# Optimization experiments

Measured on AMD Instinct MI355X. Metric: run time of the kernel, lower is better.

The kernel has to match this reference:

```python
import jax, jax.numpy as jnp
import numpy as np

N_NODES = 50000
N_EDGES = 800000
IN_F, HID, HEADS, OUT_F = 64, 64, 4, 64
NEG_SLOPE = 0.2


def _gat_conv(x, ei, W, a_src, a_dst, b, H, C):
    """PyG-style GATConv (eval mode, add_self_loops=True, concat=True).
    x: [N, F_in], ei: [2, E], W: [F_in, H*C], a_src/a_dst: [H, C], b: [H*C].
    """
    N = x.shape[0]
    h = (x @ W).reshape(N, H, C)                      # [N,H,C]
    asrc = jnp.einsum('nhc,hc->nh', h, a_src)         # [N,H]
    adst = jnp.einsum('nhc,hc->nh', h, a_dst)         # [N,H]
    src, dst = ei[0], ei[1]
    logits = jax.nn.leaky_relu(asrc[src] + adst[dst], NEG_SLOPE)  # [E,H]
    m = jax.ops.segment_max(logits, dst, num_segments=N)
    m = jnp.where(jnp.isfinite(m), m, 0.0)
    ex = jnp.exp(logits - m[dst])
    denom = jax.ops.segment_sum(ex, dst, num_segments=N)
    alpha = ex / (denom[dst] + 1e-16)                 # [E,H]
    msg = h[src] * alpha[:, :, None]                  # [E,H,C]
    out = jax.ops.segment_sum(msg, dst, num_segments=N)  # [N,H,C]
    return out.reshape(N, H * C) + b


def _add_self_loops(ei, n):
    loops = jnp.arange(n, dtype=ei.dtype)
    return jnp.concatenate([ei, jnp.stack([loops, loops])], axis=1)


def setup_inputs() -> dict:
    key = jax.random.key(0)
    ks = jax.random.split(key, 16)
    x = jax.random.normal(ks[0], (N_NODES, IN_F), dtype=jnp.float32)
    edge_index = jax.random.randint(ks[1], (2, N_EDGES), 0, N_NODES, dtype=jnp.int32)
    s = 0.1
    d = {'x': x, 'edge_index': edge_index}
    # layer 0: IN_F -> HID, HEADS heads
    d['W0'] = jax.random.normal(ks[2], (IN_F, HEADS * HID), jnp.float32) * s
    d['a_src0'] = jax.random.normal(ks[3], (HEADS, HID), jnp.float32) * s
    d['a_dst0'] = jax.random.normal(ks[4], (HEADS, HID), jnp.float32) * s
    d['b0'] = jnp.zeros((HEADS * HID,), jnp.float32)
    # layer 1: HEADS*HID -> HID, HEADS heads
    d['W1'] = jax.random.normal(ks[5], (HEADS * HID, HEADS * HID), jnp.float32) * s
    d['a_src1'] = jax.random.normal(ks[6], (HEADS, HID), jnp.float32) * s
    d['a_dst1'] = jax.random.normal(ks[7], (HEADS, HID), jnp.float32) * s
    d['b1'] = jnp.zeros((HEADS * HID,), jnp.float32)
    # layer 2: HEADS*HID -> OUT_F, 1 head
    d['W2'] = jax.random.normal(ks[8], (HEADS * HID, OUT_F), jnp.float32) * s
    d['a_src2'] = jax.random.normal(ks[9], (1, OUT_F), jnp.float32) * s
    d['a_dst2'] = jax.random.normal(ks[10], (1, OUT_F), jnp.float32) * s
    d['b2'] = jnp.zeros((OUT_F,), jnp.float32)
    return d


def reference(x, edge_index, W0, a_src0, a_dst0, b0, W1, a_src1, a_dst1, b1, W2, a_src2, a_dst2, b2):
    ei = _add_self_loops(edge_index, x.shape[0])
    h = _gat_conv(x, ei, W0, a_src0, a_dst0, b0, HEADS, HID)
    h = jax.nn.elu(h)  # dropout identity in eval
    h = _gat_conv(h, ei, W1, a_src1, a_dst1, b1, HEADS, HID)
    h = jax.nn.elu(h)
    out = _gat_conv(h, ei, W2, a_src2, a_dst2, b2, 1, OUT_F)
    return out
```

## Files before the change

kernel.cpp:

```cpp
#include <hip/hip_runtime.h>
#include <hip/hip_fp16.h>
#include <math.h>

#define NODES 50000
#define EDGES 800000
#define NB_SCAN ((NODES + 1023) / 1024)

typedef __attribute__((ext_vector_type(8))) _Float16 f16x8;
typedef __attribute__((ext_vector_type(4))) _Float16 f16x4;
typedef __attribute__((ext_vector_type(4))) float f32x4;

__device__ __forceinline__ float lrelu02(float x){ return x > 0.f ? x : 0.2f * x; }

__device__ __forceinline__ f32x4 shflx4(f32x4 v, int m){
  f32x4 r;
  r[0] = __shfl_xor(v[0], m); r[1] = __shfl_xor(v[1], m);
  r[2] = __shfl_xor(v[2], m); r[3] = __shfl_xor(v[3], m);
  return r;
}


__global__ __launch_bounds__(256) void gat_zero(int* __restrict__ p, int n){
  int i = blockIdx.x * 256 + threadIdx.x;
  if (i < n) p[i] = 0;
}

__global__ __launch_bounds__(256) void gat_hist(const int* __restrict__ ei, int* __restrict__ cnt){
  int e = blockIdx.x * 256 + threadIdx.x;
  if (e < EDGES) atomicAdd(&cnt[ei[EDGES + e]], 1);
}

__global__ __launch_bounds__(256) void gat_blocksum(const int* __restrict__ cnt, int* __restrict__ bsums){
  __shared__ int sd[256];
  int t = threadIdx.x, b = blockIdx.x;
  int base = b * 1024 + t * 4, s = 0;
  #pragma unroll
  for (int j = 0; j < 4; j++){ int i = base + j; if (i < NODES) s += cnt[i]; }
  sd[t] = s; __syncthreads();
  for (int o = 128; o > 0; o >>= 1){ if (t < o) sd[t] += sd[t + o]; __syncthreads(); }
  if (t == 0) bsums[b] = sd[0];
}

__global__ void gat_scan_bsums(int* bsums, int nb){
  if (threadIdx.x == 0 && blockIdx.x == 0){
    int run = 0;
    for (int i = 0; i < nb; i++){ int v = bsums[i]; bsums[i] = run; run += v; }
  }
}

__global__ __launch_bounds__(256) void gat_rowptr(int* __restrict__ cnt, const int* __restrict__ bsums,
                                                  int* __restrict__ row_ptr){
  __shared__ int sd[256];
  int t = threadIdx.x, b = blockIdx.x;
  int base = b * 1024 + t * 4;
  int c[4]; int s = 0;
  #pragma unroll
  for (int j = 0; j < 4; j++){
    int i = base + j;
    c[j] = (i < NODES) ? cnt[i] : 0;
    s += c[j];
    if (i < NODES) cnt[i] = 0;
  }
  sd[t] = s; __syncthreads();
  for (int o = 1; o < 256; o <<= 1){
    int v = (t >= o) ? sd[t - o] : 0;
    __syncthreads();
    if (t >= o) sd[t] += v;
    __syncthreads();
  }
  int off = bsums[b] + sd[t] - s;
  #pragma unroll
  for (int j = 0; j < 4; j++){
    int i = base + j;
    if (i < NODES){ row_ptr[i] = off; off += c[j]; }
  }
  if (b == 0 && t == 0) row_ptr[NODES] = EDGES;
}

__global__ __launch_bounds__(256) void gat_scatter(const int* __restrict__ ei, const int* __restrict__ row_ptr,
                                                    int* __restrict__ fill, int* __restrict__ col,
                                                    int* __restrict__ dstarr){
  int e = blockIdx.x * 256 + threadIdx.x;
  if (e < EDGES){
    int s = ei[e], d = ei[EDGES + e];
    int pos = row_ptr[d] + atomicAdd(&fill[d], 1);
    col[pos] = s;
    dstarr[pos] = d;
  }
}


__global__ __launch_bounds__(256) void gat_cvt_h(const float* __restrict__ src, _Float16* __restrict__ dst, int n4){
  int i = blockIdx.x * 256 + threadIdx.x;
  if (i < n4){
    float4 v = *(const float4*)(src + (size_t)i * 4);
    f16x4 h = { (_Float16)v.x, (_Float16)v.y, (_Float16)v.z, (_Float16)v.w };
    *(f16x4*)(dst + (size_t)i * 4) = h;
  }
}

__global__ __launch_bounds__(256) void gat_wt_all(const float* __restrict__ W0, const float* __restrict__ W1,
                                                  const float* __restrict__ W2,
                                                  _Float16* __restrict__ Wt0, _Float16* __restrict__ Wt1,
                                                  _Float16* __restrict__ Wt2){
  int n = threadIdx.x;
  int k = blockIdx.x;
  if (k < 64){
    Wt0[(size_t)n * 64 + k] = (_Float16)W0[(size_t)k * 256 + n];
  } else if (k < 320){
    int kk = k - 64;
    Wt1[(size_t)n * 256 + kk] = (_Float16)W1[(size_t)kk * 256 + n];
  } else {
    int kk = k - 320;
    if (n < 64) Wt2[(size_t)n * 256 + kk] = (_Float16)W2[(size_t)kk * 64 + n];
  }
}

__global__ __launch_bounds__(256) void gat_ws0(const float* __restrict__ W0, const float* __restrict__ a_src0,
                                               const float* __restrict__ a_dst0,
                                               float* __restrict__ ws, float* __restrict__ wd){
  int t = threadIdx.x;
  int h = t >> 6, c = t & 63;
  float s = 0.f, d = 0.f;
  for (int cc = 0; cc < 64; cc++){
    float w = W0[(size_t)c * 256 + h * 64 + cc];
    s += w * a_src0[h * 64 + cc];
    d += w * a_dst0[h * 64 + cc];
  }
  ws[h * 64 + c] = s;
  wd[h * 64 + c] = d;
}


template<int K, int N>
__global__ __launch_bounds__(256) void gat_gemm_mfma(const _Float16* __restrict__ A, const _Float16* __restrict__ Wt,
                                                      _Float16* __restrict__ C, int M){
  constexpr int NT = N / 64;
  constexpr int LDT = 40;
  __shared__ _Float16 As[64][LDT];
  __shared__ _Float16 Bs[N][LDT];

  int tid = threadIdx.x;
  int w = tid >> 6, l = tid & 63;
  int lg = l >> 4, lr = l & 15;
  int bm = blockIdx.x * 64;

  f32x4 acc[4][NT];
  #pragma unroll
  for (int m = 0; m < 4; m++)
    #pragma unroll
    for (int n = 0; n < NT; n++)
      acc[m][n] = (f32x4){0.f, 0.f, 0.f, 0.f};

  int ar = tid >> 2;
  int akc = (tid & 3) * 8;
  bool avalid = (bm + ar) < M;
  const _Float16* aptr = A + (size_t)(bm + ar) * K + akc;

  for (int k0 = 0; k0 < K; k0 += 32){
    float4 av = avalid ? *(const float4*)(aptr + k0) : make_float4(0.f, 0.f, 0.f, 0.f);
    __syncthreads();
    *(float4*)&As[ar][akc] = av;
    #pragma unroll
    for (int c = 0; c < N / 64; c++){
      int idx = c * 256 + tid;
      int n = idx >> 2, kc = (idx & 3) * 8;
      *(float4*)&Bs[n][kc] = *(const float4*)(Wt + (size_t)n * K + k0 + kc);
    }
    __syncthreads();

    f16x8 af[4], bf[NT];
    #pragma unroll
    for (int m = 0; m < 4; m++) af[m] = *(const f16x8*)&As[16 * m + lr][8 * lg];
    #pragma unroll
    for (int n = 0; n < NT; n++) bf[n] = *(const f16x8*)&Bs[w * (N / 4) + 16 * n + lr][8 * lg];
    #pragma unroll
    for (int m = 0; m < 4; m++)
      #pragma unroll
      for (int n = 0; n < NT; n++)
        acc[m][n] = __builtin_amdgcn_mfma_f32_16x16x32_f16(af[m], bf[n], acc[m][n], 0, 0, 0);
  }

  #pragma unroll
  for (int m = 0; m < 4; m++){
    #pragma unroll
    for (int j = 0; j < 4; j++){
      int row = bm + 16 * m + 4 * lg + j;
      if (row < M){
        #pragma unroll
        for (int n = 0; n < NT; n++)
          C[(size_t)row * N + w * (N / 4) + 16 * n + lr] = (_Float16)acc[m][n][j];
      }
    }
  }
}


__global__ __launch_bounds__(256) void gat_gemm_bd(const _Float16* __restrict__ A, const _Float16* __restrict__ Bt,
                                                    const float* __restrict__ bias, _Float16* __restrict__ C, int M){
  int tid = threadIdx.x;
  int w = tid >> 6, l = tid & 63;
  int lg = l >> 4, lr = l & 15;
  int bm = blockIdx.x * 64;

  f32x4 acc[4][4];
  #pragma unroll
  for (int m = 0; m < 4; m++)
    #pragma unroll
    for (int n = 0; n < 4; n++)
      acc[m][n] = (f32x4){0.f, 0.f, 0.f, 0.f};

  f16x8 zf = {};
  #pragma unroll
  for (int ks = 0; ks < 2; ks++){
    int koff = ks * 32;
    f16x8 af[4], bf[4];
    #pragma unroll
    for (int m = 0; m < 4; m++){
      int row = bm + 16 * m + lr;
      af[m] = (row < M) ? *(const f16x8*)(A + (size_t)row * 256 + w * 64 + koff + 8 * lg) : zf;
    }
    #pragma unroll
    for (int n = 0; n < 4; n++)
      bf[n] = *(const f16x8*)(Bt + (size_t)(w * 64 + 16 * n + lr) * 64 + koff + 8 * lg);
    #pragma unroll
    for (int m = 0; m < 4; m++)
      #pragma unroll
      for (int n = 0; n < 4; n++)
        acc[m][n] = __builtin_amdgcn_mfma_f32_16x16x32_f16(af[m], bf[n], acc[m][n], 0, 0, 0);
  }

  #pragma unroll
  for (int m = 0; m < 4; m++){
    #pragma unroll
    for (int j = 0; j < 4; j++){
      int row = bm + 16 * m + 4 * lg + j;
      if (row < M){
        #pragma unroll
        for (int n = 0; n < 4; n++){
          int cc = w * 64 + 16 * n + lr;
          float o = acc[m][n][j] + bias[cc];
          o = o > 0.f ? o : expm1f(o);
          C[(size_t)row * 256 + cc] = (_Float16)o;
        }
      }
    }
  }
}


__global__ __launch_bounds__(256) void gat_attn0(const _Float16* __restrict__ xh, const float* __restrict__ ws,
                                                  const float* __restrict__ wd,
                                                  float* __restrict__ asrc, float* __restrict__ adst, int N){
  int lane = threadIdx.x & 63;
  int wid = threadIdx.x >> 6;
  int n = blockIdx.x * 4 + wid;
  if (n >= N) return;
  float v = (float)xh[(size_t)n * 64 + lane];
  #pragma unroll
  for (int h = 0; h < 4; h++){
    float s1 = v * ws[h * 64 + lane];
    float s2 = v * wd[h * 64 + lane];
    #pragma unroll
    for (int o = 32; o > 0; o >>= 1){ s1 += __shfl_xor(s1, o); s2 += __shfl_xor(s2, o); }
    if (lane == 0){ asrc[n * 4 + h] = s1; adst[n * 4 + h] = s2; }
  }
}

__global__ __launch_bounds__(256) void gat_attn4(const _Float16* __restrict__ h, const float* __restrict__ a_src,
                                                  const float* __restrict__ a_dst,
                                                  float* __restrict__ asrc, float* __restrict__ adst, int N){
  int lane = threadIdx.x & 63;
  int wid = threadIdx.x >> 6;
  int n = blockIdx.x * 4 + wid;
  if (n >= N) return;
  int co = lane * 4;
  f16x4 hv = *(const f16x4*)(h + (size_t)n * 256 + co);
  float4 av = *(const float4*)&a_src[co];
  float4 dv = *(const float4*)&a_dst[co];
  float f0 = (float)hv[0], f1 = (float)hv[1], f2 = (float)hv[2], f3 = (float)hv[3];
  float s1 = f0 * av.x + f1 * av.y + f2 * av.z + f3 * av.w;
  float s2 = f0 * dv.x + f1 * dv.y + f2 * dv.z + f3 * dv.w;
  #pragma unroll
  for (int o = 8; o > 0; o >>= 1){ s1 += __shfl_xor(s1, o); s2 += __shfl_xor(s2, o); }
  if ((lane & 15) == 0){
    int q = lane >> 4;
    asrc[n * 4 + q] = s1;
    adst[n * 4 + q] = s2;
  }
}

__global__ __launch_bounds__(256) void gat_attn1(const _Float16* __restrict__ h, const float* __restrict__ a_src,
                                                  const float* __restrict__ a_dst,
                                                  float* __restrict__ asrc, float* __restrict__ adst, int N){
  int lane = threadIdx.x & 63;
  int wid = threadIdx.x >> 6;
  int n = blockIdx.x * 4 + wid;
  if (n >= N) return;
  float v = (float)h[(size_t)n * 64 + lane];
  float s1 = v * a_src[lane];
  float s2 = v * a_dst[lane];
  #pragma unroll
  for (int o = 32; o > 0; o >>= 1){ s1 += __shfl_xor(s1, o); s2 += __shfl_xor(s2, o); }
  if (lane == 0){ asrc[n] = s1; adst[n] = s2; }
}


__global__ __launch_bounds__(256) void gat_edge_exp0(const int* __restrict__ col, const int* __restrict__ dstarr,
                                                      const float* __restrict__ asrc, const float* __restrict__ adst,
                                                      float* __restrict__ exf){
  int i = blockIdx.x * 256 + threadIdx.x;
  if (i >= EDGES) return;
  int s = col[i], d = dstarr[i];
  float4 a = *(const float4*)&asrc[s * 4];
  float4 b = *(const float4*)&adst[d * 4];
  float4 r;
  r.x = __expf(lrelu02(a.x + b.x));
  r.y = __expf(lrelu02(a.y + b.y));
  r.z = __expf(lrelu02(a.z + b.z));
  r.w = __expf(lrelu02(a.w + b.w));
  *(float4*)&exf[(size_t)i * 4] = r;
}

__global__ __launch_bounds__(256) void gat_edge_exp1h(const int* __restrict__ col, const int* __restrict__ dstarr,
                                                       const float* __restrict__ asrc, const float* __restrict__ adst,
                                                       float* __restrict__ exf1){
  int i = blockIdx.x * 256 + threadIdx.x;
  if (i >= EDGES) return;
  exf1[i] = __expf(lrelu02(asrc[col[i]] + adst[dstarr[i]]));
}


__global__ __launch_bounds__(256) void gat_aggregate_in64(const _Float16* __restrict__ xh, const float* __restrict__ exf,
                                                           const float* __restrict__ asrc, const float* __restrict__ adst,
                                                           const int* __restrict__ row_ptr, const int* __restrict__ col,
                                                           _Float16* __restrict__ agg){
  int lane = threadIdx.x & 63;
  int wid = threadIdx.x >> 6;
  int d = blockIdx.x * 4 + wid;
  if (d >= NODES) return;
  int slot = lane >> 4;
  int cpos = (lane & 15) * 4;

  f32x4 acc0 = {0,0,0,0}, acc1 = {0,0,0,0}, acc2 = {0,0,0,0}, acc3 = {0,0,0,0};
  f32x4 den = {0,0,0,0};

  int e0 = row_ptr[d], e1 = row_ptr[d + 1];
  const _Float16* xb = xh + cpos;
  int e = e0;
  for (; e + 8 <= e1; e += 8){
    int eA = e + slot, eB = e + 4 + slot;
    int sA = col[eA], sB = col[eB];
    float4 fA = *(const float4*)(exf + (size_t)eA * 4);
    float4 fB = *(const float4*)(exf + (size_t)eB * 4);
    f16x4 hA = *(const f16x4*)(xb + (size_t)sA * 64);
    f16x4 hB = *(const f16x4*)(xb + (size_t)sB * 64);
    f32x4 vA = { (float)hA[0], (float)hA[1], (float)hA[2], (float)hA[3] };
    f32x4 vB = { (float)hB[0], (float)hB[1], (float)hB[2], (float)hB[3] };
    den += (f32x4){ fA.x + fB.x, fA.y + fB.y, fA.z + fB.z, fA.w + fB.w };
    acc0 += fA.x * vA + fB.x * vB;
    acc1 += fA.y * vA + fB.y * vB;
    acc2 += fA.z * vA + fB.z * vB;
    acc3 += fA.w * vA + fB.w * vB;
  }
  if (e + 4 <= e1){
    int eA = e + slot;
    int sA = col[eA];
    float4 fA = *(const float4*)(exf + (size_t)eA * 4);
    f16x4 hA = *(const f16x4*)(xb + (size_t)sA * 64);
    f32x4 vA = { (float)hA[0], (float)hA[1], (float)hA[2], (float)hA[3] };
    den += (f32x4){ fA.x, fA.y, fA.z, fA.w };
    acc0 += fA.x * vA; acc1 += fA.y * vA; acc2 += fA.z * vA; acc3 += fA.w * vA;
    e += 4;
  }
  {
    int eA = e + slot;
    if (eA < e1){
      int sA = col[eA];
      float4 fA = *(const float4*)(exf + (size_t)eA * 4);
      f16x4 hA = *(const f16x4*)(xb + (size_t)sA * 64);
      f32x4 vA = { (float)hA[0], (float)hA[1], (float)hA[2], (float)hA[3] };
      den += (f32x4){ fA.x, fA.y, fA.z, fA.w };
      acc0 += fA.x * vA; acc1 += fA.y * vA; acc2 += fA.z * vA; acc3 += fA.w * vA;
    }
  }

  #pragma unroll
  for (int off = 16; off <= 32; off <<= 1){
    acc0 += shflx4(acc0, off);
    acc1 += shflx4(acc1, off);
    acc2 += shflx4(acc2, off);
    acc3 += shflx4(acc3, off);
    den  += shflx4(den,  off);
  }

  float4 a4 = *(const float4*)&asrc[d * 4];
  float4 b4 = *(const float4*)&adst[d * 4];
  float es0 = __expf(lrelu02(a4.x + b4.x));
  float es1 = __expf(lrelu02(a4.y + b4.y));
  float es2 = __expf(lrelu02(a4.z + b4.z));
  float es3 = __expf(lrelu02(a4.w + b4.w));
  f16x4 hs = *(const f16x4*)(xh + (size_t)d * 64 + cpos);
  f32x4 vs = { (float)hs[0], (float)hs[1], (float)hs[2], (float)hs[3] };
  acc0 += es0 * vs; acc1 += es1 * vs; acc2 += es2 * vs; acc3 += es3 * vs;
  den += (f32x4){ es0, es1, es2, es3 };

  if (slot == 0){
    float i0 = 1.f / (den[0] + 1e-16f), i1 = 1.f / (den[1] + 1e-16f);
    float i2 = 1.f / (den[2] + 1e-16f), i3 = 1.f / (den[3] + 1e-16f);
    _Float16* ob = agg + (size_t)d * 256 + cpos;
    f16x4 o0 = { (_Float16)(acc0[0]*i0), (_Float16)(acc0[1]*i0), (_Float16)(acc0[2]*i0), (_Float16)(acc0[3]*i0) };
    f16x4 o1 = { (_Float16)(acc1[0]*i1), (_Float16)(acc1[1]*i1), (_Float16)(acc1[2]*i1), (_Float16)(acc1[3]*i1) };
    f16x4 o2 = { (_Float16)(acc2[0]*i2), (_Float16)(acc2[1]*i2), (_Float16)(acc2[2]*i2), (_Float16)(acc2[3]*i2) };
    f16x4 o3 = { (_Float16)(acc3[0]*i3), (_Float16)(acc3[1]*i3), (_Float16)(acc3[2]*i3), (_Float16)(acc3[3]*i3) };
    *(f16x4*)(ob)       = o0;
    *(f16x4*)(ob + 64)  = o1;
    *(f16x4*)(ob + 128) = o2;
    *(f16x4*)(ob + 192) = o3;
  }
}


__global__ __launch_bounds__(256) void gat_aggregate4(const _Float16* __restrict__ hH, const float* __restrict__ asrc,
                                                       const float* __restrict__ adst,
                                                       const int* __restrict__ row_ptr, const int* __restrict__ col,
                                                       const float* __restrict__ bias, _Float16* __restrict__ out){
  int lane = threadIdx.x & 63;
  int wid = threadIdx.x >> 6;
  int d = blockIdx.x * 4 + wid;
  if (d >= NODES) return;
  int q = lane >> 4;
  int co = lane * 4;

  float adq = adst[d * 4 + q];

  float ex = __expf(lrelu02(asrc[d * 4 + q] + adq));
  f16x4 hv = *(const f16x4*)(hH + (size_t)d * 256 + co);
  float4 acc = make_float4(ex * (float)hv[0], ex * (float)hv[1], ex * (float)hv[2], ex * (float)hv[3]);
  float den = ex;

  int e0 = row_ptr[d], e1 = row_ptr[d + 1];
  const _Float16* hbase = hH + co;
  int e = e0;
  for (; e < e1 && (e & 3); e++){
    int s0 = col[e];
    float a0 = asrc[s0 * 4 + q];
    f16x4 h0 = *(const f16x4*)(hbase + (size_t)s0 * 256);
    float x0 = __expf(lrelu02(a0 + adq));
    den += x0;
    acc.x += x0 * (float)h0[0]; acc.y += x0 * (float)h0[1];
    acc.z += x0 * (float)h0[2]; acc.w += x0 * (float)h0[3];
  }
  for (; e + 8 <= e1; e += 8){
    int4 cA = *(const int4*)&col[e];
    int4 cB = *(const int4*)&col[e + 4];
    float a0 = asrc[cA.x * 4 + q], a1 = asrc[cA.y * 4 + q], a2 = asrc[cA.z * 4 + q], a3 = asrc[cA.w * 4 + q];
    float a4 = asrc[cB.x * 4 + q], a5 = asrc[cB.y * 4 + q], a6 = asrc[cB.z * 4 + q], a7 = asrc[cB.w * 4 + q];
    f16x4 h0 = *(const f16x4*)(hbase + (size_t)cA.x * 256);
    f16x4 h1 = *(const f16x4*)(hbase + (size_t)cA.y * 256);
    f16x4 h2 = *(const f16x4*)(hbase + (size_t)cA.z * 256);
    f16x4 h3 = *(const f16x4*)(hbase + (size_t)cA.w * 256);
    f16x4 h4 = *(const f16x4*)(hbase + (size_t)cB.x * 256);
    f16x4 h5 = *(const f16x4*)(hbase + (size_t)cB.y * 256);
    f16x4 h6 = *(const f16x4*)(hbase + (size_t)cB.z * 256);
    f16x4 h7 = *(const f16x4*)(hbase + (size_t)cB.w * 256);
    float x0 = __expf(lrelu02(a0 + adq)), x1 = __expf(lrelu02(a1 + adq));
    float x2 = __expf(lrelu02(a2 + adq)), x3 = __expf(lrelu02(a3 + adq));
    float x4 = __expf(lrelu02(a4 + adq)), x5 = __expf(lrelu02(a5 + adq));
    float x6 = __expf(lrelu02(a6 + adq)), x7 = __expf(lrelu02(a7 + adq));
    den += x0 + x1 + x2 + x3 + x4 + x5 + x6 + x7;
    acc.x += x0 * (float)h0[0] + x1 * (float)h1[0] + x2 * (float)h2[0] + x3 * (float)h3[0]
           + x4 * (float)h4[0] + x5 * (float)h5[0] + x6 * (float)h6[0] + x7 * (float)h7[0];
    acc.y += x0 * (float)h0[1] + x1 * (float)h1[1] + x2 * (float)h2[1] + x3 * (float)h3[1]
           + x4 * (float)h4[1] + x5 * (float)h5[1] + x6 * (float)h6[1] + x7 * (float)h7[1];
    acc.z += x0 * (float)h0[2] + x1 * (float)h1[2] + x2 * (float)h2[2] + x3 * (float)h3[2]
           + x4 * (float)h4[2] + x5 * (float)h5[2] + x6 * (float)h6[2] + x7 * (float)h7[2];
    acc.w += x0 * (float)h0[3] + x1 * (float)h1[3] + x2 * (float)h2[3] + x3 * (float)h3[3]
           + x4 * (float)h4[3] + x5 * (float)h5[3] + x6 * (float)h6[3] + x7 * (float)h7[3];
  }
  for (; e < e1; e++){
    int s0 = col[e];
    float a0 = asrc[s0 * 4 + q];
    f16x4 h0 = *(const f16x4*)(hbase + (size_t)s0 * 256);
    float x0 = __expf(lrelu02(a0 + adq));
    den += x0;
    acc.x += x0 * (float)h0[0]; acc.y += x0 * (float)h0[1];
    acc.z += x0 * (float)h0[2]; acc.w += x0 * (float)h0[3];
  }

  float inv = 1.f / (den + 1e-16f);
  float4 b4 = *(const float4*)&bias[co];
  float4 o = make_float4(acc.x * inv + b4.x, acc.y * inv + b4.y, acc.z * inv + b4.z, acc.w * inv + b4.w);
  o.x = o.x > 0.f ? o.x : expm1f(o.x);
  o.y = o.y > 0.f ? o.y : expm1f(o.y);
  o.z = o.z > 0.f ? o.z : expm1f(o.z);
  o.w = o.w > 0.f ? o.w : expm1f(o.w);
  f16x4 oh = { (_Float16)o.x, (_Float16)o.y, (_Float16)o.z, (_Float16)o.w };
  *(f16x4*)(out + (size_t)d * 256 + co) = oh;
}


__global__ __launch_bounds__(256) void gat_aggregate1n(const _Float16* __restrict__ hH, const float* __restrict__ exf1,
                                                        const float* __restrict__ asrc, const float* __restrict__ adst,
                                                        const int* __restrict__ row_ptr, const int* __restrict__ col,
                                                        const float* __restrict__ bias, float* __restrict__ out){
  int lane = threadIdx.x & 63;
  int wid = threadIdx.x >> 6;
  int d = blockIdx.x * 4 + wid;
  if (d >= NODES) return;
  int slot = lane >> 4;
  int cpos = (lane & 15) * 4;

  f32x4 acc = {0,0,0,0};
  float den = 0.f;

  int e0 = row_ptr[d], e1 = row_ptr[d + 1];
  const _Float16* hb = hH + cpos;
  int e = e0;
  for (; e + 8 <= e1; e += 8){
    int eA = e + slot, eB = e + 4 + slot;
    int sA = col[eA], sB = col[eB];
    float fA = exf1[eA], fB = exf1[eB];
    f16x4 hA = *(const f16x4*)(hb + (size_t)sA * 64);
    f16x4 hB = *(const f16x4*)(hb + (size_t)sB * 64);
    f32x4 vA = { (float)hA[0], (float)hA[1], (float)hA[2], (float)hA[3] };
    f32x4 vB = { (float)hB[0], (float)hB[1], (float)hB[2], (float)hB[3] };
    den += fA + fB;
    acc += fA * vA + fB * vB;
  }
  if (e + 4 <= e1){
    int eA = e + slot;
    int sA = col[eA];
    float fA = exf1[eA];
    f16x4 hA = *(const f16x4*)(hb + (size_t)sA * 64);
    f32x4 vA = { (float)hA[0], (float)hA[1], (float)hA[2], (float)hA[3] };
    den += fA; acc += fA * vA;
    e += 4;
  }
  {
    int eA = e + slot;
    if (eA < e1){
      int sA = col[eA];
      float fA = exf1[eA];
      f16x4 hA = *(const f16x4*)(hb + (size_t)sA * 64);
      f32x4 vA = { (float)hA[0], (float)hA[1], (float)hA[2], (float)hA[3] };
      den += fA; acc += fA * vA;
    }
  }

  #pragma unroll
  for (int off = 16; off <= 32; off <<= 1){
    acc += shflx4(acc, off);
    den += __shfl_xor(den, off);
  }

  float es = __expf(lrelu02(asrc[d] + adst[d]));
  f16x4 hs = *(const f16x4*)(hH + (size_t)d * 64 + cpos);
  f32x4 vs = { (float)hs[0], (float)hs[1], (float)hs[2], (float)hs[3] };
  acc += es * vs;
  den += es;

  if (slot == 0){
    float inv = 1.f / (den + 1e-16f);
    float4 b4 = *(const float4*)&bias[cpos];
    float4 o = make_float4(acc[0] * inv + b4.x, acc[1] * inv + b4.y, acc[2] * inv + b4.z, acc[3] * inv + b4.w);
    *(float4*)(out + (size_t)d * 64 + cpos) = o;
  }
}


extern "C" void kernel_launch(void* const* d_in, const int* in_sizes, int n_in,
                              void* d_out, int out_size, void* d_ws, size_t ws_size,
                              hipStream_t stream) {
  const float* x   = (const float*)d_in[0];
  const int*   ei  = (const int*)  d_in[1];
  const float* W0  = (const float*)d_in[2];
  const float* as0 = (const float*)d_in[3];
  const float* ad0 = (const float*)d_in[4];
  const float* b0  = (const float*)d_in[5];
  const float* W1  = (const float*)d_in[6];
  const float* as1 = (const float*)d_in[7];
  const float* ad1 = (const float*)d_in[8];
  const float* b1  = (const float*)d_in[9];
  const float* W2  = (const float*)d_in[10];
  const float* as2 = (const float*)d_in[11];
  const float* ad2 = (const float*)d_in[12];
  const float* b2  = (const float*)d_in[13];
  float* out = (float*)d_out;

  auto al = [](size_t v){ return (v + 255) & ~(size_t)255; };
  char* p = (char*)d_ws;
  int*      row_ptr = (int*)p;      p += al((NODES + 1) * sizeof(int));
  int*      cnt     = (int*)p;      p += al(NODES * sizeof(int));
  int*      bsums   = (int*)p;      p += al(64 * sizeof(int));
  int*      col     = (int*)p;      p += al(EDGES * sizeof(int));
  int*      dstarr  = (int*)p;      p += al(EDGES * sizeof(int));
  float*    exf     = (float*)p;    p += al((size_t)EDGES * 4 * sizeof(float));
  float*    asrc    = (float*)p;    p += al(NODES * 4 * sizeof(float));
  float*    adst    = (float*)p;    p += al(NODES * 4 * sizeof(float));
  _Float16* xh      = (_Float16*)p; p += al((size_t)NODES * 64 * sizeof(_Float16));
  _Float16* hH      = (_Float16*)p; p += al((size_t)NODES * 256 * sizeof(_Float16));
  _Float16* actb    = (_Float16*)p; p += al((size_t)NODES * 256 * sizeof(_Float16));
  _Float16* Wt0     = (_Float16*)p; p += al(256 * 64 * sizeof(_Float16));
  _Float16* Wt1     = (_Float16*)p; p += al(256 * 256 * sizeof(_Float16));
  _Float16* Wt2     = (_Float16*)p; p += al(64 * 256 * sizeof(_Float16));
  float*    ws0     = (float*)p;    p += al(256 * sizeof(float));
  float*    wd0     = (float*)p;    p += al(256 * sizeof(float));

  gat_cvt_h<<<(NODES * 64 / 4 + 255) / 256, 256, 0, stream>>>(x, xh, NODES * 64 / 4);
  gat_wt_all<<<576, 256, 0, stream>>>(W0, W1, W2, Wt0, Wt1, Wt2);
  gat_ws0<<<1, 256, 0, stream>>>(W0, as0, ad0, ws0, wd0);

  gat_zero<<<(NODES + 255) / 256, 256, 0, stream>>>(cnt, NODES);
  gat_hist<<<(EDGES + 255) / 256, 256, 0, stream>>>(ei, cnt);
  gat_blocksum<<<NB_SCAN, 256, 0, stream>>>(cnt, bsums);
  gat_scan_bsums<<<1, 64, 0, stream>>>(bsums, NB_SCAN);
  gat_rowptr<<<NB_SCAN, 256, 0, stream>>>(cnt, bsums, row_ptr);
  gat_scatter<<<(EDGES + 255) / 256, 256, 0, stream>>>(ei, row_ptr, cnt, col, dstarr);

  const int nodeBlocks = (NODES + 3) / 4;
  const int gemmBlocks = (NODES + 63) / 64;
  const int edgeBlocks = (EDGES + 255) / 256;

  gat_attn0<<<nodeBlocks, 256, 0, stream>>>(xh, ws0, wd0, asrc, adst, NODES);
  gat_edge_exp0<<<edgeBlocks, 256, 0, stream>>>(col, dstarr, asrc, adst, exf);
  gat_aggregate_in64<<<nodeBlocks, 256, 0, stream>>>(xh, exf, asrc, adst, row_ptr, col, hH);
  gat_gemm_bd<<<gemmBlocks, 256, 0, stream>>>(hH, Wt0, b0, actb, NODES);

  gat_gemm_mfma<256, 256><<<gemmBlocks, 256, 0, stream>>>(actb, Wt1, hH, NODES);
  gat_attn4<<<nodeBlocks, 256, 0, stream>>>(hH, as1, ad1, asrc, adst, NODES);
  gat_aggregate4<<<nodeBlocks, 256, 0, stream>>>(hH, asrc, adst, row_ptr, col, b1, actb);

  gat_gemm_mfma<256, 64><<<gemmBlocks, 256, 0, stream>>>(actb, Wt2, hH, NODES);
  gat_attn1<<<nodeBlocks, 256, 0, stream>>>(hH, as2, ad2, asrc, adst, NODES);
  gat_edge_exp1h<<<edgeBlocks, 256, 0, stream>>>(col, dstarr, asrc, adst, exf);
  gat_aggregate1n<<<nodeBlocks, 256, 0, stream>>>(hH, exf, asrc, adst, row_ptr, col, b2, out);
}
```

Before: 373.4 us.

## Fuse attention-score projections into GEMM epilogues and merge prep kernels

Computes the per-node source/destination attention scores for layers 1 and 2 inside the MFMA GEMM epilogue from the fp32 accumulators. This removes the separate attn4/attn1 kernels that re-read the GEMM output. The layer-2 edge-exp kernel is dropped and the exponentials are computed inline in the final aggregation. The three prep kernels are merged into one launch, and the layer-1 aggregation loop is simplified to a 4-wide unroll without alignment handling, which reduces memory-level parallelism per iteration.

```diff
diff --git a/kernel.cpp b/kernel.cpp
--- a/kernel.cpp
+++ b/kernel.cpp
@@ -90,51 +90,50 @@
 }
 
 
-__global__ __launch_bounds__(256) void gat_cvt_h(const float* __restrict__ src, _Float16* __restrict__ dst, int n4){
-  int i = blockIdx.x * 256 + threadIdx.x;
-  if (i < n4){
-    float4 v = *(const float4*)(src + (size_t)i * 4);
+__global__ __launch_bounds__(256) void gat_prep(const float* __restrict__ x, _Float16* __restrict__ xh,
+                                                const float* __restrict__ W0, const float* __restrict__ W1,
+                                                const float* __restrict__ W2,
+                                                _Float16* __restrict__ Wt0, _Float16* __restrict__ Wt1,
+                                                _Float16* __restrict__ Wt2,
+                                                const float* __restrict__ as0, const float* __restrict__ ad0,
+                                                float* __restrict__ ws, float* __restrict__ wd){
+  int b = blockIdx.x;
+  int t = threadIdx.x;
+  if (b < 3125){
+    int i = b * 256 + t;
+    float4 v = *(const float4*)(x + (size_t)i * 4);
     f16x4 h = { (_Float16)v.x, (_Float16)v.y, (_Float16)v.z, (_Float16)v.w };
-    *(f16x4*)(dst + (size_t)i * 4) = h;
-  }
-}
-
-__global__ __launch_bounds__(256) void gat_wt_all(const float* __restrict__ W0, const float* __restrict__ W1,
-                                                  const float* __restrict__ W2,
-                                                  _Float16* __restrict__ Wt0, _Float16* __restrict__ Wt1,
-                                                  _Float16* __restrict__ Wt2){
-  int n = threadIdx.x;
-  int k = blockIdx.x;
-  if (k < 64){
-    Wt0[(size_t)n * 64 + k] = (_Float16)W0[(size_t)k * 256 + n];
-  } else if (k < 320){
-    int kk = k - 64;
-    Wt1[(size_t)n * 256 + kk] = (_Float16)W1[(size_t)kk * 256 + n];
+    *(f16x4*)(xh + (size_t)i * 4) = h;
+  } else if (b < 3701){
+    int k = b - 3125;
+    if (k < 64){
+      Wt0[(size_t)t * 64 + k] = (_Float16)W0[(size_t)k * 256 + t];
+    } else if (k < 320){
+      int kk = k - 64;
+      Wt1[(size_t)t * 256 + kk] = (_Float16)W1[(size_t)kk * 256 + t];
+    } else {
+      int kk = k - 320;
+      if (t < 64) Wt2[(size_t)t * 256 + kk] = (_Float16)W2[(size_t)kk * 64 + t];
+    }
   } else {
-    int kk = k - 320;
-    if (n < 64) Wt2[(size_t)n * 256 + kk] = (_Float16)W2[(size_t)kk * 64 + n];
-  }
-}
-
-__global__ __launch_bounds__(256) void gat_ws0(const float* __restrict__ W0, const float* __restrict__ a_src0,
-                                               const float* __restrict__ a_dst0,
-                                               float* __restrict__ ws, float* __restrict__ wd){
-  int t = threadIdx.x;
-  int h = t >> 6, c = t & 63;
-  float s = 0.f, d = 0.f;
-  for (int cc = 0; cc < 64; cc++){
-    float w = W0[(size_t)c * 256 + h * 64 + cc];
-    s += w * a_src0[h * 64 + cc];
-    d += w * a_dst0[h * 64 + cc];
-  }
-  ws[h * 64 + c] = s;
-  wd[h * 64 + c] = d;
-}
-
-
-template<int K, int N>
+    int h = t >> 6, c = t & 63;
+    float s = 0.f, d = 0.f;
+    for (int cc = 0; cc < 64; cc++){
+      float w = W0[(size_t)c * 256 + h * 64 + cc];
+      s += w * as0[h * 64 + cc];
+      d += w * ad0[h * 64 + cc];
+    }
+    ws[h * 64 + c] = s;
+    wd[h * 64 + c] = d;
+  }
+}
+
+
+template<int K, int N, int ATTN>
 __global__ __launch_bounds__(256) void gat_gemm_mfma(const _Float16* __restrict__ A, const _Float16* __restrict__ Wt,
-                                                      _Float16* __restrict__ C, int M){
+                                                      _Float16* __restrict__ C,
+                                                      const float* __restrict__ a_srcv, const float* __restrict__ a_dstv,
+                                                      float* __restrict__ asrc, float* __restrict__ adst, int M){
   constexpr int NT = N / 64;
   constexpr int LDT = 40;
   __shared__ _Float16 As[64][LDT];
@@ -190,6 +189,56 @@
         #pragma unroll
         for (int n = 0; n < NT; n++)
           C[(size_t)row * N + w * (N / 4) + 16 * n + lr] = (_Float16)acc[m][n][j];
+      }
+    }
+  }
+
+  if constexpr (ATTN == 4){
+    float avs[4], avd[4];
+    #pragma unroll
+    for (int n = 0; n < 4; n++){
+      avs[n] = a_srcv[w * 64 + 16 * n + lr];
+      avd[n] = a_dstv[w * 64 + 16 * n + lr];
+    }
+    #pragma unroll
+    for (int m = 0; m < 4; m++){
+      #pragma unroll
+      for (int j = 0; j < 4; j++){
+        float s1 = acc[m][0][j] * avs[0] + acc[m][1][j] * avs[1] + acc[m][2][j] * avs[2] + acc[m][3][j] * avs[3];
+        float s2 = acc[m][0][j] * avd[0] + acc[m][1][j] * avd[1] + acc[m][2][j] * avd[2] + acc[m][3][j] * avd[3];
+        #pragma unroll
+        for (int o = 8; o > 0; o >>= 1){ s1 += __shfl_xor(s1, o); s2 += __shfl_xor(s2, o); }
+        int row = bm + 16 * m + 4 * lg + j;
+        if (lr == 0 && row < M){
+          asrc[row * 4 + w] = s1;
+          adst[row * 4 + w] = s2;
+        }
+      }
+    }
+  }
+  if constexpr (ATTN == 1){
+    __shared__ float sred[2][4][64];
+    float av = a_srcv[w * 16 + lr], dv = a_dstv[w * 16 + lr];
+    #pragma unroll
+    for (int m = 0; m < 4; m++){
+      #pragma unroll
+      for (int j = 0; j < 4; j++){
+        float s1 = acc[m][0][j] * av;
+        float s2 = acc[m][0][j] * dv;
+        #pragma unroll
+        for (int o = 8; o > 0; o >>= 1){ s1 += __shfl_xor(s1, o); s2 += __shfl_xor(s2, o); }
+        if (lr == 0){
+          sred[0][w][16 * m + 4 * lg + j] = s1;
+          sred[1][w][16 * m + 4 * lg + j] = s2;
+        }
+      }
+    }
+    __syncthreads();
+    if (tid < 64){
+      int row = bm + tid;
+      if (row < M){
+        asrc[row] = sred[0][0][tid] + sred[0][1][tid] + sred[0][2][tid] + sred[0][3][tid];
+        adst[row] = sred[1][0][tid] + sred[1][1][tid] + sred[1][2][tid] + sred[1][3][tid];
       }
     }
   }
@@ -265,44 +314,6 @@
     for (int o = 32; o > 0; o >>= 1){ s1 += __shfl_xor(s1, o); s2 += __shfl_xor(s2, o); }
     if (lane == 0){ asrc[n * 4 + h] = s1; adst[n * 4 + h] = s2; }
   }
-}
-
-__global__ __launch_bounds__(256) void gat_attn4(const _Float16* __restrict__ h, const float* __restrict__ a_src,
-                                                  const float* __restrict__ a_dst,
-                                                  float* __restrict__ asrc, float* __restrict__ adst, int N){
-  int lane = threadIdx.x & 63;
-  int wid = threadIdx.x >> 6;
-  int n = blockIdx.x * 4 + wid;
-  if (n >= N) return;
-  int co = lane * 4;
-  f16x4 hv = *(const f16x4*)(h + (size_t)n * 256 + co);
-  float4 av = *(const float4*)&a_src[co];
-  float4 dv = *(const float4*)&a_dst[co];
-  float f0 = (float)hv[0], f1 = (float)hv[1], f2 = (float)hv[2], f3 = (float)hv[3];
-  float s1 = f0 * av.x + f1 * av.y + f2 * av.z + f3 * av.w;
-  float s2 = f0 * dv.x + f1 * dv.y + f2 * dv.z + f3 * dv.w;
-  #pragma unroll
-  for (int o = 8; o > 0; o >>= 1){ s1 += __shfl_xor(s1, o); s2 += __shfl_xor(s2, o); }
-  if ((lane & 15) == 0){
-    int q = lane >> 4;
-    asrc[n * 4 + q] = s1;
-    adst[n * 4 + q] = s2;
-  }
-}
-
-__global__ __launch_bounds__(256) void gat_attn1(const _Float16* __restrict__ h, const float* __restrict__ a_src,
-                                                  const float* __restrict__ a_dst,
-                                                  float* __restrict__ asrc, float* __restrict__ adst, int N){
-  int lane = threadIdx.x & 63;
-  int wid = threadIdx.x >> 6;
-  int n = blockIdx.x * 4 + wid;
-  if (n >= N) return;
-  float v = (float)h[(size_t)n * 64 + lane];
-  float s1 = v * a_src[lane];
-  float s2 = v * a_dst[lane];
-  #pragma unroll
-  for (int o = 32; o > 0; o >>= 1){ s1 += __shfl_xor(s1, o); s2 += __shfl_xor(s2, o); }
-  if (lane == 0){ asrc[n] = s1; adst[n] = s2; }
 }
 
 
@@ -320,14 +331,6 @@
   r.z = __expf(lrelu02(a.z + b.z));
   r.w = __expf(lrelu02(a.w + b.w));
   *(float4*)&exf[(size_t)i * 4] = r;
-}
-
-__global__ __launch_bounds__(256) void gat_edge_exp1h(const int* __restrict__ col, const int* __restrict__ dstarr,
-                                                       const float* __restrict__ asrc, const float* __restrict__ adst,
-                                                       float* __restrict__ exf1){
-  int i = blockIdx.x * 256 + threadIdx.x;
-  if (i >= EDGES) return;
-  exf1[i] = __expf(lrelu02(asrc[col[i]] + adst[dstarr[i]]));
 }
 
 
@@ -442,41 +445,22 @@
   int e0 = row_ptr[d], e1 = row_ptr[d + 1];
   const _Float16* hbase = hH + co;
   int e = e0;
-  for (; e < e1 && (e & 3); e++){
-    int s0 = col[e];
-    float a0 = asrc[s0 * 4 + q];
+  for (; e + 4 <= e1; e += 4){
+    int s0 = col[e], s1 = col[e + 1], s2 = col[e + 2], s3 = col[e + 3];
+    float a0 = asrc[s0 * 4 + q], a1 = asrc[s1 * 4 + q], a2 = asrc[s2 * 4 + q], a3 = asrc[s3 * 4 + q];
     f16x4 h0 = *(const f16x4*)(hbase + (size_t)s0 * 256);
+    f16x4 h1 = *(const f16x4*)(hbase + (size_t)s1 * 256);
+    f16x4 h2 = *(const f16x4*)(hbase + (size_t)s2 * 256);
+    f16x4 h3 = *(const f16x4*)(hbase + (size_t)s3 * 256);
     float x0 = __expf(lrelu02(a0 + adq));
-    den += x0;
-    acc.x += x0 * (float)h0[0]; acc.y += x0 * (float)h0[1];
-    acc.z += x0 * (float)h0[2]; acc.w += x0 * (float)h0[3];
-  }
-  for (; e + 8 <= e1; e += 8){
-    int4 cA = *(const int4*)&col[e];
-    int4 cB = *(const int4*)&col[e + 4];
-    float a0 = asrc[cA.x * 4 + q], a1 = asrc[cA.y * 4 + q], a2 = asrc[cA.z * 4 + q], a3 = asrc[cA.w * 4 + q];
-    float a4 = asrc[cB.x * 4 + q], a5 = asrc[cB.y * 4 + q], a6 = asrc[cB.z * 4 + q], a7 = asrc[cB.w * 4 + q];
-    f16x4 h0 = *(const f16x4*)(hbase + (size_t)cA.x * 256);
-    f16x4 h1 = *(const f16x4*)(hbase + (size_t)cA.y * 256);
-    f16x4 h2 = *(const f16x4*)(hbase + (size_t)cA.z * 256);
-    f16x4 h3 = *(const f16x4*)(hbase + (size_t)cA.w * 256);
-    f16x4 h4 = *(const f16x4*)(hbase + (size_t)cB.x * 256);
-    f16x4 h5 = *(const f16x4*)(hbase + (size_t)cB.y * 256);
-    f16x4 h6 = *(const f16x4*)(hbase + (size_t)cB.z * 256);
-    f16x4 h7 = *(const f16x4*)(hbase + (size_t)cB.w * 256);
-    float x0 = __expf(lrelu02(a0 + adq)), x1 = __expf(lrelu02(a1 + adq));
-    float x2 = __expf(lrelu02(a2 + adq)), x3 = __expf(lrelu02(a3 + adq));
-    float x4 = __expf(lrelu02(a4 + adq)), x5 = __expf(lrelu02(a5 + adq));
-    float x6 = __expf(lrelu02(a6 + adq)), x7 = __expf(lrelu02(a7 + adq));
-    den += x0 + x1 + x2 + x3 + x4 + x5 + x6 + x7;
-    acc.x += x0 * (float)h0[0] + x1 * (float)h1[0] + x2 * (float)h2[0] + x3 * (float)h3[0]
-           + x4 * (float)h4[0] + x5 * (float)h5[0] + x6 * (float)h6[0] + x7 * (float)h7[0];
-    acc.y += x0 * (float)h0[1] + x1 * (float)h1[1] + x2 * (float)h2[1] + x3 * (float)h3[1]
-           + x4 * (float)h4[1] + x5 * (float)h5[1] + x6 * (float)h6[1] + x7 * (float)h7[1];
-    acc.z += x0 * (float)h0[2] + x1 * (float)h1[2] + x2 * (float)h2[2] + x3 * (float)h3[2]
-           + x4 * (float)h4[2] + x5 * (float)h5[2] + x6 * (float)h6[2] + x7 * (float)h7[2];
-    acc.w += x0 * (float)h0[3] + x1 * (float)h1[3] + x2 * (float)h2[3] + x3 * (float)h3[3]
-           + x4 * (float)h4[3] + x5 * (float)h5[3] + x6 * (float)h6[3] + x7 * (float)h7[3];
+    float x1 = __expf(lrelu02(a1 + adq));
+    float x2 = __expf(lrelu02(a2 + adq));
+    float x3 = __expf(lrelu02(a3 + adq));
+    den += x0 + x1 + x2 + x3;
+    acc.x += x0 * (float)h0[0] + x1 * (float)h1[0] + x2 * (float)h2[0] + x3 * (float)h3[0];
+    acc.y += x0 * (float)h0[1] + x1 * (float)h1[1] + x2 * (float)h2[1] + x3 * (float)h3[1];
+    acc.z += x0 * (float)h0[2] + x1 * (float)h1[2] + x2 * (float)h2[2] + x3 * (float)h3[2];
+    acc.w += x0 * (float)h0[3] + x1 * (float)h1[3] + x2 * (float)h2[3] + x3 * (float)h3[3];
   }
   for (; e < e1; e++){
     int s0 = col[e];
@@ -500,7 +484,7 @@
 }
 
 
-__global__ __launch_bounds__(256) void gat_aggregate1n(const _Float16* __restrict__ hH, const float* __restrict__ exf1,
+__global__ __launch_bounds__(256) void gat_aggregate1n(const _Float16* __restrict__ hH,
                                                         const float* __restrict__ asrc, const float* __restrict__ adst,
                                                         const int* __restrict__ row_ptr, const int* __restrict__ col,
                                                         const float* __restrict__ bias, float* __restrict__ out){
@@ -511,6 +495,7 @@
   int slot = lane >> 4;
   int cpos = (lane & 15) * 4;
 
+  float adq = adst[d];
   f32x4 acc = {0,0,0,0};
   float den = 0.f;
 
@@ -520,7 +505,8 @@
   for (; e + 8 <= e1; e += 8){
     int eA = e + slot, eB = e + 4 + slot;
     int sA = col[eA], sB = col[eB];
-    float fA = exf1[eA], fB = exf1[eB];
+    float fA = __expf(lrelu02(asrc[sA] + adq));
+    float fB = __expf(lrelu02(asrc[sB] + adq));
     f16x4 hA = *(const f16x4*)(hb + (size_t)sA * 64);
     f16x4 hB = *(const f16x4*)(hb + (size_t)sB * 64);
     f32x4 vA = { (float)hA[0], (float)hA[1], (float)hA[2], (float)hA[3] };
@@ -531,7 +517,7 @@
   if (e + 4 <= e1){
     int eA = e + slot;
     int sA = col[eA];
-    float fA = exf1[eA];
+    float fA = __expf(lrelu02(asrc[sA] + adq));
     f16x4 hA = *(const f16x4*)(hb + (size_t)sA * 64);
     f32x4 vA = { (float)hA[0], (float)hA[1], (float)hA[2], (float)hA[3] };
     den += fA; acc += fA * vA;
@@ -541,7 +527,7 @@
     int eA = e + slot;
     if (eA < e1){
       int sA = col[eA];
-      float fA = exf1[eA];
+      float fA = __expf(lrelu02(asrc[sA] + adq));
       f16x4 hA = *(const f16x4*)(hb + (size_t)sA * 64);
       f32x4 vA = { (float)hA[0], (float)hA[1], (float)hA[2], (float)hA[3] };
       den += fA; acc += fA * vA;
@@ -554,7 +540,7 @@
     den += __shfl_xor(den, off);
   }
 
-  float es = __expf(lrelu02(asrc[d] + adst[d]));
+  float es = __expf(lrelu02(asrc[d] + adq));
   f16x4 hs = *(const f16x4*)(hH + (size_t)d * 64 + cpos);
   f32x4 vs = { (float)hs[0], (float)hs[1], (float)hs[2], (float)hs[3] };
   acc += es * vs;
@@ -607,9 +593,7 @@
   float*    ws0     = (float*)p;    p += al(256 * sizeof(float));
   float*    wd0     = (float*)p;    p += al(256 * sizeof(float));
 
-  gat_cvt_h<<<(NODES * 64 / 4 + 255) / 256, 256, 0, stream>>>(x, xh, NODES * 64 / 4);
-  gat_wt_all<<<576, 256, 0, stream>>>(W0, W1, W2, Wt0, Wt1, Wt2);
-  gat_ws0<<<1, 256, 0, stream>>>(W0, as0, ad0, ws0, wd0);
+  gat_prep<<<3702, 256, 0, stream>>>(x, xh, W0, W1, W2, Wt0, Wt1, Wt2, as0, ad0, ws0, wd0);
 
   gat_zero<<<(NODES + 255) / 256, 256, 0, stream>>>(cnt, NODES);
   gat_hist<<<(EDGES + 255) / 256, 256, 0, stream>>>(ei, cnt);
@@ -627,12 +611,9 @@
   gat_aggregate_in64<<<nodeBlocks, 256, 0, stream>>>(xh, exf, asrc, adst, row_ptr, col, hH);
   gat_gemm_bd<<<gemmBlocks, 256, 0, stream>>>(hH, Wt0, b0, actb, NODES);
 
-  gat_gemm_mfma<256, 256><<<gemmBlocks, 256, 0, stream>>>(actb, Wt1, hH, NODES);
-  gat_attn4<<<nodeBlocks, 256, 0, stream>>>(hH, as1, ad1, asrc, adst, NODES);
+  gat_gemm_mfma<256, 256, 4><<<gemmBlocks, 256, 0, stream>>>(actb, Wt1, hH, as1, ad1, asrc, adst, NODES);
   gat_aggregate4<<<nodeBlocks, 256, 0, stream>>>(hH, asrc, adst, row_ptr, col, b1, actb);
 
-  gat_gemm_mfma<256, 64><<<gemmBlocks, 256, 0, stream>>>(actb, Wt2, hH, NODES);
-  gat_attn1<<<nodeBlocks, 256, 0, stream>>>(hH, as2, ad2, asrc, adst, NODES);
-  gat_edge_exp1h<<<edgeBlocks, 256, 0, stream>>>(col, dstarr, asrc, adst, exf);
-  gat_aggregate1n<<<nodeBlocks, 256, 0, stream>>>(hH, exf, asrc, adst, row_ptr, col, b2, out);
-}
+  gat_gemm_mfma<256, 64, 1><<<gemmBlocks, 256, 0, stream>>>(actb, Wt2, hH, as2, ad2, asrc, adst, NODES);
+  gat_aggregate1n<<<nodeBlocks, 256, 0, stream>>>(hH, asrc, adst, row_ptr, col, b2, out);
+}
```

Result: faster. 347.1 us (-7.0%).
